# Kernel tuning notes

Hardware: AMD Instinct MI355X
Metric: run time of the kernel (lower is better)

## Reference

```python
import jax, jax.numpy as jnp
import numpy as np

B, INPUT_DIM, HEAD = 16384, 1024, 8
DIM = INPUT_DIM // HEAD


def setup_inputs() -> dict:
    key = jax.random.key(0)
    k1, k2, kw1, kb1, kw2, kw3 = jax.random.split(key, 6)
    x1 = jax.random.normal(k1, (B, INPUT_DIM), dtype=jnp.float32)
    x2 = jax.random.normal(k2, (B, INPUT_DIM), dtype=jnp.float32)
    s = 1.0 / np.sqrt(DIM)
    W1 = jax.random.uniform(kw1, (HEAD, DIM), jnp.float32, -s, s)   # per-head Linear(dim,1) weight
    b1 = jax.random.uniform(kb1, (HEAD,), jnp.float32, -s, s)       # per-head Linear(dim,1) bias
    W2 = jax.random.uniform(kw2, (HEAD, DIM), jnp.float32, -s, s)   # per-head Linear(dim,1,bias=False)
    W3 = jax.random.uniform(kw3, (HEAD, DIM, DIM), jnp.float32, -s, s)  # per-head Linear(dim,dim) [out,in]
    return {"x1": x1, "x2": x2, "W1": W1, "b1": b1, "W2": W2, "W3": W3}


def reference(x1, x2, W1, b1, W2, W3):
    b = x1.shape[0]
    h1 = x1.reshape(b, HEAD, DIM)
    h2 = x2.reshape(b, HEAD, DIM)
    # per-head scalar linears: [b, head]
    t1 = jnp.einsum('bhd,hd->bh', h1, W1) + b1
    t2 = jnp.einsum('bhd,hd->bh', h2, W2)
    # diag(w3(x1_h) @ x2_h^T) == sum((x1_h @ W3_h^T) * x2_h, -1), batched over heads
    proj = jnp.einsum('bhi,hoi->bho', h1, W3)
    t3 = jnp.sum(proj * h2, axis=-1)
    return jnp.sum(t1 + t2 + t3, axis=1)  # [b]
```

## Files before the change

### kernel.cpp

```cpp
#include <hip/hip_runtime.h>


#define NB 16384
#define NHEAD 8
#define NDIM 128

typedef __attribute__((ext_vector_type(8))) short bf16x8;
typedef __attribute__((ext_vector_type(4))) float f32x4;

__global__ __launch_bounds__(256) void prep_w3(
    const float* __restrict__ W3, short* __restrict__ whi,
    short* __restrict__ wlo)
{
    const int t    = blockIdx.x * 256 + threadIdx.x;
    const int lane = t & 63;
    const int nt   = (t >> 6) & 7;
    const int kk   = (t >> 9) & 3;
    const int h    = t >> 11;
    const int lm   = lane & 15;
    const int lg   = lane >> 4;

    const float* src = W3 + ((size_t)(h * NDIM + nt * 16 + lm)) * NDIM
                          + kk * 32 + lg * 8;
    const float4 a = *reinterpret_cast<const float4*>(src);
    const float4 b = *reinterpret_cast<const float4*>(src + 4);
    float xf[8] = {a.x, a.y, a.z, a.w, b.x, b.y, b.z, b.w};
    bf16x8 hi, lo;
#pragma unroll
    for (int j = 0; j < 8; ++j) {
        const unsigned u = __float_as_uint(xf[j]);
        hi[j] = (short)(u >> 16);
        const float hf = __uint_as_float(u & 0xffff0000u);
        lo[j] = (short)(__float_as_uint(xf[j] - hf) >> 16);
    }
    reinterpret_cast<bf16x8*>(whi)[t] = hi;
    reinterpret_cast<bf16x8*>(wlo)[t] = lo;
}

__global__ __launch_bounds__(256, 4) void bilinear_mfma(
    const float* __restrict__ x1, const float* __restrict__ x2,
    const float* __restrict__ W1, const float* __restrict__ W2,
    const short* __restrict__ whi, const short* __restrict__ wlo,
    float* __restrict__ psum)
{
    const int tid = threadIdx.x;
    const int w   = tid >> 6;
    const int l   = tid & 63;
    const int lm  = l & 15;
    const int lg  = l >> 4;
    const int bid = blockIdx.x;
    const int h   = bid & 7;
    const int b0  = (bid >> 3) * 64;
    const int bw  = b0 + w * 16;

    __shared__ short lhi[2][4096];
    __shared__ short llo[2][4096];

    const float4* __restrict__ shi = reinterpret_cast<const float4*>(
        whi + (size_t)h * 16384);
    const float4* __restrict__ slo = reinterpret_cast<const float4*>(
        wlo + (size_t)h * 16384);

    const float* __restrict__ w1base = W1 + h * NDIM;
    const float* __restrict__ x1base = x1 + (size_t)(bw + lm) * (NHEAD * NDIM)
                                          + h * NDIM + lg * 8;

    f32x4 acc[8];
#pragma unroll
    for (int nt = 0; nt < 8; ++nt) acc[nt] = (f32x4)0.f;
    float t1 = 0.f;

    {
        const float4 a0 = shi[tid];
        const float4 a1 = shi[tid + 256];
        const float4 c0 = slo[tid];
        const float4 c1 = slo[tid + 256];
        reinterpret_cast<float4*>(&lhi[0][0])[0 + tid]   = a0;
        reinterpret_cast<float4*>(&lhi[0][0])[256 + tid] = a1;
        reinterpret_cast<float4*>(&llo[0][0])[0 + tid]   = c0;
        reinterpret_cast<float4*>(&llo[0][0])[256 + tid] = c1;
    }
    float4 pa = *reinterpret_cast<const float4*>(x1base);
    float4 pb = *reinterpret_cast<const float4*>(x1base + 4);
    __syncthreads();

#pragma unroll
    for (int kk = 0; kk < 4; ++kk) {
        const int cur = kk & 1;
        const int nxt = (kk + 1) & 1;

        float4 nh0, nh1, nl0, nl1;
        if (kk < 3) {
            nh0 = shi[(kk + 1) * 512 + tid];
            nh1 = shi[(kk + 1) * 512 + tid + 256];
            nl0 = slo[(kk + 1) * 512 + tid];
            nl1 = slo[(kk + 1) * 512 + tid + 256];
        }
        const float4 ca = pa, cb = pb;
        if (kk < 3) {
            pa = *reinterpret_cast<const float4*>(x1base + (kk + 1) * 32);
            pb = *reinterpret_cast<const float4*>(x1base + (kk + 1) * 32 + 4);
        }

        bf16x8 ahi, alo;
        {
            const int k0 = kk * 32 + lg * 8;
            const float4 wa = *reinterpret_cast<const float4*>(w1base + k0);
            const float4 wb = *reinterpret_cast<const float4*>(w1base + k0 + 4);
            float xf[8]  = {ca.x, ca.y, ca.z, ca.w, cb.x, cb.y, cb.z, cb.w};
            float w1f[8] = {wa.x, wa.y, wa.z, wa.w, wb.x, wb.y, wb.z, wb.w};
#pragma unroll
            for (int j = 0; j < 8; ++j) {
                const unsigned u = __float_as_uint(xf[j]);
                ahi[j] = (short)(u >> 16);
                const float hf = __uint_as_float(u & 0xffff0000u);
                alo[j] = (short)(__float_as_uint(xf[j] - hf) >> 16);
                t1 += xf[j] * w1f[j];
            }
        }

#pragma unroll
        for (int nt = 0; nt < 8; ++nt) {
            const bf16x8 bhi = *reinterpret_cast<const bf16x8*>(
                &lhi[cur][nt * 512 + l * 8]);
            const bf16x8 blo = *reinterpret_cast<const bf16x8*>(
                &llo[cur][nt * 512 + l * 8]);
            acc[nt] = __builtin_amdgcn_mfma_f32_16x16x32_bf16(ahi, bhi, acc[nt], 0, 0, 0);
            acc[nt] = __builtin_amdgcn_mfma_f32_16x16x32_bf16(alo, bhi, acc[nt], 0, 0, 0);
            acc[nt] = __builtin_amdgcn_mfma_f32_16x16x32_bf16(ahi, blo, acc[nt], 0, 0, 0);
        }

        if (kk < 3) {
            reinterpret_cast<float4*>(&lhi[nxt][0])[0 + tid]   = nh0;
            reinterpret_cast<float4*>(&lhi[nxt][0])[256 + tid] = nh1;
            reinterpret_cast<float4*>(&llo[nxt][0])[0 + tid]   = nl0;
            reinterpret_cast<float4*>(&llo[nxt][0])[256 + tid] = nl1;
        }
        __syncthreads();
    }

    float w2v[8];
#pragma unroll
    for (int nt = 0; nt < 8; ++nt) w2v[nt] = W2[h * NDIM + nt * 16 + lm];

    float cr[4];
#pragma unroll
    for (int r = 0; r < 4; ++r) {
        const float* x2p = x2 + (size_t)(bw + lg * 4 + r) * (NHEAD * NDIM)
                            + h * NDIM + lm;
        float s = 0.f;
#pragma unroll
        for (int nt = 0; nt < 8; ++nt)
            s += (acc[nt][r] + w2v[nt]) * x2p[nt * 16];
        cr[r] = s;
    }
#pragma unroll
    for (int m = 1; m < 16; m <<= 1)
#pragma unroll
        for (int r = 0; r < 4; ++r) cr[r] += __shfl_xor(cr[r], m, 64);

    float tf = t1;
    tf += __shfl_xor(tf, 16, 64);
    tf += __shfl_xor(tf, 32, 64);
#pragma unroll
    for (int r = 0; r < 4; ++r) cr[r] += __shfl(tf, lg * 4 + r, 64);

    if (lm == 0) {
        float4 st;
        st.x = cr[0]; st.y = cr[1]; st.z = cr[2]; st.w = cr[3];
        *reinterpret_cast<float4*>(&psum[(size_t)h * NB + bw + lg * 4]) = st;
    }
}

__global__ __launch_bounds__(256) void bilinear_reduce(
    const float* __restrict__ psum, const float* __restrict__ b1,
    float* __restrict__ out)
{
    const int i = blockIdx.x * 256 + threadIdx.x;
    float bs = 0.f;
#pragma unroll
    for (int hh = 0; hh < NHEAD; ++hh) bs += b1[hh];
    float s = bs;
#pragma unroll
    for (int hh = 0; hh < NHEAD; ++hh) s += psum[(size_t)hh * NB + i];
    out[i] = s;
}

extern "C" void kernel_launch(void* const* d_in, const int* in_sizes, int n_in,
                              void* d_out, int out_size, void* d_ws, size_t ws_size,
                              hipStream_t stream) {
    const float* x1 = (const float*)d_in[0];
    const float* x2 = (const float*)d_in[1];
    const float* W1 = (const float*)d_in[2];
    const float* b1 = (const float*)d_in[3];
    const float* W2 = (const float*)d_in[4];
    const float* W3 = (const float*)d_in[5];
    float* out = (float*)d_out;

    short* whi = (short*)d_ws;
    short* wlo = whi + (size_t)NHEAD * NDIM * NDIM;
    float* psum = (float*)((char*)d_ws + 512 * 1024);

    prep_w3<<<dim3(64), dim3(256), 0, stream>>>(W3, whi, wlo);
    bilinear_mfma<<<dim3(NB / 64 * NHEAD), dim3(256), 0, stream>>>(
        x1, x2, W1, W2, whi, wlo, psum);
    bilinear_reduce<<<dim3(NB / 256), dim3(256), 0, stream>>>(psum, b1, out);
}
```

Before: 35.85 us.

## Stream W3 tiles directly into LDS and prefetch x2 early

Replaces the register-staged global-to-LDS copy of the bf16 W3 hi/lo tiles with direct global_load_lds transfers, removing the VGPR round-trip and the LDS store instructions. It also loads all x2 values needed for the epilogue into registers at kernel start, so their latency overlaps the MFMA loop. In exchange it holds 32 extra registers per thread, which may reduce occupancy. It also relies on correct wait handling for the asynchronous LDS loads before each barrier.

```diff
diff --git a/kernel.cpp b/kernel.cpp
--- a/kernel.cpp
+++ b/kernel.cpp
@@ -7,6 +7,12 @@
 
 typedef __attribute__((ext_vector_type(8))) short bf16x8;
 typedef __attribute__((ext_vector_type(4))) float f32x4;
+
+__device__ __forceinline__ void gload_lds16(const void* g, void* l) {
+    __builtin_amdgcn_global_load_lds(
+        (const __attribute__((address_space(1))) unsigned*)g,
+        (__attribute__((address_space(3))) unsigned*)l, 16, 0, 0);
+}
 
 __global__ __launch_bounds__(256) void prep_w3(
     const float* __restrict__ W3, short* __restrict__ whi,
@@ -56,45 +62,50 @@
     __shared__ short lhi[2][4096];
     __shared__ short llo[2][4096];
 
-    const float4* __restrict__ shi = reinterpret_cast<const float4*>(
-        whi + (size_t)h * 16384);
-    const float4* __restrict__ slo = reinterpret_cast<const float4*>(
-        wlo + (size_t)h * 16384);
+    const short* __restrict__ shi = whi + (size_t)h * 16384;
+    const short* __restrict__ slo = wlo + (size_t)h * 16384;
 
     const float* __restrict__ w1base = W1 + h * NDIM;
     const float* __restrict__ x1base = x1 + (size_t)(bw + lm) * (NHEAD * NDIM)
                                           + h * NDIM + lg * 8;
 
+    float x2r[4][8];
+    {
+        const float* x2base = x2 + (size_t)(bw + lg * 4) * (NHEAD * NDIM)
+                                 + h * NDIM + lm;
+#pragma unroll
+        for (int r = 0; r < 4; ++r)
+#pragma unroll
+            for (int nt = 0; nt < 8; ++nt)
+                x2r[r][nt] = x2base[(size_t)r * (NHEAD * NDIM) + nt * 16];
+    }
+
+    gload_lds16(shi + (size_t)(tid) * 8,        &lhi[0][(w * 64) * 8]);
+    gload_lds16(shi + (size_t)(256 + tid) * 8,  &lhi[0][(256 + w * 64) * 8]);
+    gload_lds16(slo + (size_t)(tid) * 8,        &llo[0][(w * 64) * 8]);
+    gload_lds16(slo + (size_t)(256 + tid) * 8,  &llo[0][(256 + w * 64) * 8]);
+
+    float4 pa = *reinterpret_cast<const float4*>(x1base);
+    float4 pb = *reinterpret_cast<const float4*>(x1base + 4);
+
     f32x4 acc[8];
 #pragma unroll
     for (int nt = 0; nt < 8; ++nt) acc[nt] = (f32x4)0.f;
     float t1 = 0.f;
 
-    {
-        const float4 a0 = shi[tid];
-        const float4 a1 = shi[tid + 256];
-        const float4 c0 = slo[tid];
-        const float4 c1 = slo[tid + 256];
-        reinterpret_cast<float4*>(&lhi[0][0])[0 + tid]   = a0;
-        reinterpret_cast<float4*>(&lhi[0][0])[256 + tid] = a1;
-        reinterpret_cast<float4*>(&llo[0][0])[0 + tid]   = c0;
-        reinterpret_cast<float4*>(&llo[0][0])[256 + tid] = c1;
-    }
-    float4 pa = *reinterpret_cast<const float4*>(x1base);
-    float4 pb = *reinterpret_cast<const float4*>(x1base + 4);
     __syncthreads();
 
 #pragma unroll
     for (int kk = 0; kk < 4; ++kk) {
         const int cur = kk & 1;
-        const int nxt = (kk + 1) & 1;
-
-        float4 nh0, nh1, nl0, nl1;
+        const int nxt = cur ^ 1;
+
         if (kk < 3) {
-            nh0 = shi[(kk + 1) * 512 + tid];
-            nh1 = shi[(kk + 1) * 512 + tid + 256];
-            nl0 = slo[(kk + 1) * 512 + tid];
-            nl1 = slo[(kk + 1) * 512 + tid + 256];
+            const size_t g0 = (size_t)((kk + 1) * 512 + tid) * 8;
+            gload_lds16(shi + g0,            &lhi[nxt][(w * 64) * 8]);
+            gload_lds16(shi + g0 + 256 * 8,  &lhi[nxt][(256 + w * 64) * 8]);
+            gload_lds16(slo + g0,            &llo[nxt][(w * 64) * 8]);
+            gload_lds16(slo + g0 + 256 * 8,  &llo[nxt][(256 + w * 64) * 8]);
         }
         const float4 ca = pa, cb = pb;
         if (kk < 3) {
@@ -130,12 +141,6 @@
             acc[nt] = __builtin_amdgcn_mfma_f32_16x16x32_bf16(ahi, blo, acc[nt], 0, 0, 0);
         }
 
-        if (kk < 3) {
-            reinterpret_cast<float4*>(&lhi[nxt][0])[0 + tid]   = nh0;
-            reinterpret_cast<float4*>(&lhi[nxt][0])[256 + tid] = nh1;
-            reinterpret_cast<float4*>(&llo[nxt][0])[0 + tid]   = nl0;
-            reinterpret_cast<float4*>(&llo[nxt][0])[256 + tid] = nl1;
-        }
         __syncthreads();
     }
 
@@ -146,12 +151,10 @@
     float cr[4];
 #pragma unroll
     for (int r = 0; r < 4; ++r) {
-        const float* x2p = x2 + (size_t)(bw + lg * 4 + r) * (NHEAD * NDIM)
-                            + h * NDIM + lm;
         float s = 0.f;
 #pragma unroll
         for (int nt = 0; nt < 8; ++nt)
-            s += (acc[nt][r] + w2v[nt]) * x2p[nt * 16];
+            s += (acc[nt][r] + w2v[nt]) * x2r[r][nt];
         cr[r] = s;
     }
 #pragma unroll
```

New measurement: 38.21 us. 1.07x slower.
